# Kernel tuning notes

Measured on AMD Instinct MI355X. Metric: run time of the kernel, lower is better.

Reference implementation:

```python
import jax, jax.numpy as jnp
import numpy as np

N_NODES = 100000
N_EDGES = 3200000
F_IN = 128
NOUT = 32


def _lin(x, W, b):
    return x @ W + b


def _spect_conv(x, src, dst, W, b, n_nodes):
    # edge_attr is all-ones with a single frequency (K=1), so SpectConv reduces to
    # an unweighted scatter-add of linearly transformed source-node features.
    h = x @ W                                   # [N, nout]
    agg = jax.ops.segment_sum(h[src], dst, num_segments=n_nodes)  # [N, nout]
    return agg + b


def setup_inputs() -> dict:
    key = jax.random.key(0)
    ks = jax.random.split(key, 32)
    s = 0.05

    def w(k, shape):
        return jax.random.normal(k, shape, dtype=jnp.float32) * s

    inp = {
        "x": jax.random.normal(ks[0], (N_NODES, F_IN), dtype=jnp.float32),
        "edge_index": jax.random.randint(ks[1], (2, N_EDGES), 0, N_NODES, dtype=jnp.int32),
        # SpectConv weights (single frequency) + biases
        "Wc1": w(ks[2], (F_IN, NOUT)), "bc1": jnp.zeros((NOUT,), jnp.float32),
        "Wc2": w(ks[3], (NOUT, NOUT)), "bc2": jnp.zeros((NOUT,), jnp.float32),
        "Wc3": w(ks[4], (NOUT, NOUT)), "bc3": jnp.zeros((NOUT,), jnp.float32),
        # dense branch weights
        "W11": w(ks[5], (F_IN, NOUT)), "b11": w(ks[6], (NOUT,)),
        "W12": w(ks[7], (F_IN, NOUT)), "b12": w(ks[8], (NOUT,)),
        "W13": w(ks[9], (F_IN, NOUT)), "b13": w(ks[10], (NOUT,)),
        "W21": w(ks[11], (NOUT, NOUT)), "b21": w(ks[12], (NOUT,)),
        "W22": w(ks[13], (NOUT, NOUT)), "b22": w(ks[14], (NOUT,)),
        "W23": w(ks[15], (NOUT, NOUT)), "b23": w(ks[16], (NOUT,)),
        "W31": w(ks[17], (NOUT, NOUT)), "b31": w(ks[18], (NOUT,)),
        "W32": w(ks[19], (NOUT, NOUT)), "b32": w(ks[20], (NOUT,)),
        "W33": w(ks[21], (NOUT, NOUT)), "b33": w(ks[22], (NOUT,)),
        "W2": w(ks[23], (NOUT, 1)), "b2": w(ks[24], (1,)),
    }
    return inp


def reference(x, edge_index,
              Wc1, bc1, Wc2, bc2, Wc3, bc3,
              W11, b11, W12, b12, W13, b13,
              W21, b21, W22, b22, W23, b23,
              W31, b31, W32, b32, W33, b33,
              W2, b2):
    src, dst = edge_index[0], edge_index[1]
    n = x.shape[0]
    relu = jax.nn.relu

    def block(h, Wa, ba, Wc, bc, Wm1, bm1, Wm2, bm2):
        return (relu(_lin(h, Wa, ba))
                + relu(_spect_conv(h, src, dst, Wc, bc, n))
                + relu(_lin(h, Wm1, bm1) * _lin(h, Wm2, bm2)))

    h = block(x, W11, b11, Wc1, bc1, W12, b12, W13, b13)
    h = block(h, W21, b21, Wc2, bc2, W22, b22, W23, b23)
    h = block(h, W31, b31, Wc3, bc3, W32, b32, W33, b33)
    return _lin(h, W2, b2)
```

## Files before the change

kernel.cpp:

```cpp
#include <hip/hip_runtime.h>
#include <hip/hip_bf16.h>

#define N_FEAT 32
#define CBITS 7
#define CAP   6000
#define TILE  8192

typedef __attribute__((ext_vector_type(8))) short short8;
typedef __attribute__((ext_vector_type(4))) short short4e;
typedef __attribute__((ext_vector_type(4))) float floatx4;

static __device__ __forceinline__ unsigned short f2b(float f) {
    unsigned u = __float_as_uint(f);
    return (unsigned short)((u + 0x7FFFu + ((u >> 16) & 1u)) >> 16);
}
static __device__ __forceinline__ float b2f(unsigned short b) {
    return __uint_as_float(((unsigned)b) << 16);
}

template <int K, bool BF16_IN>
__global__ __launch_bounds__(256)
void transform_mfma_kernel(const void* __restrict__ hin,
                           const float* __restrict__ Wa, const float* __restrict__ ba,
                           const float* __restrict__ Wc,
                           const float* __restrict__ Wm1, const float* __restrict__ bm1,
                           const float* __restrict__ Wm2, const float* __restrict__ bm2,
                           unsigned short* __restrict__ t_pre, unsigned short* __restrict__ t_c,
                           int n_nodes)
{
    constexpr int WPITCH = (K == 32) ? 40 : 136;
    __shared__ unsigned short sW[128][WPITCH];

    const int t = threadIdx.x;
    const int node0 = blockIdx.x * 64;
    const int wave = t >> 6;
    const int lane = t & 63;
    const int m16 = lane & 15;
    const int quad = lane >> 4;

    for (int i = t; i < 128 * K; i += 256) {
        const int c = i & 127, kk = i >> 7;
        const int mat = c >> 5, cl = c & 31;
        const float* W = (mat == 0) ? Wa : (mat == 1) ? Wc : (mat == 2) ? Wm1 : Wm2;
        sW[c][kk] = f2b(W[(size_t)kk * 32 + cl]);
    }
    __syncthreads();

    const int n = node0 + wave * 16 + m16;
    const bool nok = (n < n_nodes);

    floatx4 acc[8];
#pragma unroll
    for (int i = 0; i < 8; ++i) acc[i] = (floatx4){0.f, 0.f, 0.f, 0.f};

#pragma unroll
    for (int k0 = 0; k0 < K; k0 += 32) {
        short8 a;
        if (BF16_IN) {
            const unsigned short* hb = (const unsigned short*)hin;
            a = nok ? *reinterpret_cast<const short8*>(hb + (size_t)n * K + k0 + quad * 8)
                    : (short8){0,0,0,0,0,0,0,0};
        } else {
            const float* hf = (const float*)hin;
            if (nok) {
                const float4 v0 = *reinterpret_cast<const float4*>(hf + (size_t)n * K + k0 + quad * 8);
                const float4 v1 = *reinterpret_cast<const float4*>(hf + (size_t)n * K + k0 + quad * 8 + 4);
                union { short8 v; unsigned short u[8]; } pk;
                pk.u[0] = f2b(v0.x); pk.u[1] = f2b(v0.y); pk.u[2] = f2b(v0.z); pk.u[3] = f2b(v0.w);
                pk.u[4] = f2b(v1.x); pk.u[5] = f2b(v1.y); pk.u[6] = f2b(v1.z); pk.u[7] = f2b(v1.w);
                a = pk.v;
            } else {
                a = (short8){0,0,0,0,0,0,0,0};
            }
        }
#pragma unroll
        for (int t8 = 0; t8 < 8; ++t8) {
            const short8 b = *reinterpret_cast<const short8*>(&sW[t8 * 16 + m16][k0 + quad * 8]);
            acc[t8] = __builtin_amdgcn_mfma_f32_16x16x32_bf16(a, b, acc[t8], 0, 0, 0);
        }
    }

#pragma unroll
    for (int r = 0; r < 4; ++r) {
        const int node = node0 + wave * 16 + quad * 4 + r;
        if (node < n_nodes) {
#pragma unroll
            for (int half = 0; half < 2; ++half) {
                const int c = m16 + half * 16;
                const float av  = acc[0 + half][r] + ba[c];
                const float wcv = acc[2 + half][r];
                const float m1  = acc[4 + half][r] + bm1[c];
                const float m2  = acc[6 + half][r] + bm2[c];
                t_pre[(size_t)node * N_FEAT + c] = f2b(fmaxf(av, 0.f) + fmaxf(m1 * m2, 0.f));
                t_c[(size_t)node * N_FEAT + c] = f2b(wcv);
            }
        }
    }
}

__global__ __launch_bounds__(1024)
void coarse_bin_kernel(const int* __restrict__ src, const int* __restrict__ dst,
                       unsigned* __restrict__ cnt_g, unsigned* __restrict__ binned,
                       int n_edges, int n_buckets)
{
    __shared__ unsigned sorted[TILE];
    __shared__ unsigned short buck[TILE];
    __shared__ unsigned hist[1024];
    __shared__ unsigned lbase[1024];
    __shared__ unsigned gofs[1024];
    __shared__ unsigned wsum[16], woff[16];

    const int t = threadIdx.x;
    const int wave = t >> 6, lane = t & 63;
    const int e0 = blockIdx.x * TILE;
    const int cnt = min(TILE, n_edges - e0);
    if (cnt <= 0) return;

    hist[t] = 0;
    __syncthreads();

    unsigned dv[TILE / 1024], sv[TILE / 1024];
    int nk = 0;
    for (int i = t; i < cnt; i += 1024, ++nk) {
        dv[nk] = (unsigned)dst[e0 + i];
        sv[nk] = (unsigned)src[e0 + i];
        atomicAdd(&hist[dv[nk] >> CBITS], 1u);
    }
    __syncthreads();

    const unsigned myh = hist[t];
    if (t < n_buckets)
        gofs[t] = myh ? atomicAdd(&cnt_g[t], myh) : 0u;

    unsigned v = myh;
#pragma unroll
    for (int off = 1; off < 64; off <<= 1) {
        const unsigned nv = __shfl_up(v, off);
        if (lane >= off) v += nv;
    }
    if (lane == 63) wsum[wave] = v;
    __syncthreads();
    if (t < 16) {
        unsigned s = wsum[t];
#pragma unroll
        for (int off = 1; off < 16; off <<= 1) {
            const unsigned nv = __shfl_up(s, off, 16);
            if (t >= off) s += nv;
        }
        woff[t] = s - wsum[t];
    }
    hist[t] = 0;
    __syncthreads();
    const unsigned lb_mine = v + woff[wave] - myh;
    lbase[t] = lb_mine;
    __syncthreads();

    for (int k = 0; k < nk; ++k) {
        const unsigned b = dv[k] >> CBITS;
        const unsigned pos = lbase[b] + atomicAdd(&hist[b], 1u);
        sorted[pos] = ((dv[k] & ((1u << CBITS) - 1)) << 17) | sv[k];
        buck[pos] = (unsigned short)b;
    }
    __syncthreads();

    for (int p = t; p < cnt; p += 1024) {
        const unsigned b = buck[p];
        const unsigned gp = gofs[b] + ((unsigned)p - lbase[b]);
        if (gp < CAP) binned[(size_t)b * CAP + gp] = sorted[p];
    }
}

__global__ __launch_bounds__(512)
void fine_sort_kernel(const unsigned* __restrict__ binned,
                      const unsigned* __restrict__ cnt_g,
                      unsigned* __restrict__ total_ctr,
                      int* __restrict__ srcs,
                      unsigned* __restrict__ rowstart, unsigned* __restrict__ rowend,
                      int n_nodes, int n_buckets)
{
    __shared__ int sorted_src[CAP];
    __shared__ unsigned hist[512];
    __shared__ unsigned incl[512];
    __shared__ unsigned ebase[512];
    __shared__ unsigned wsum[8], woff[8];
    __shared__ unsigned ob_s;

    const int t = threadIdx.x;
    const int wave = t >> 6, lane = t & 63;
    const int b = blockIdx.x;
    const unsigned cnt = min(cnt_g[b], (unsigned)CAP);
    const int node0 = b << CBITS;
    const int nodes_here = min(128, n_nodes - node0);
    const unsigned* tile = binned + (size_t)b * CAP;

    if (t == 0) ob_s = atomicAdd(total_ctr, cnt);
    hist[t] = 0;
    __syncthreads();
    const unsigned ob = ob_s;

    for (unsigned i = t; i < cnt; i += 512) {
        const unsigned e = tile[i];
        atomicAdd(&hist[((e >> 17) << 2) | ((e & 0x1FFFFu) >> 15)], 1u);
    }
    __syncthreads();

    const unsigned myh = hist[t];
    unsigned v = myh;
#pragma unroll
    for (int off = 1; off < 64; off <<= 1) {
        const unsigned nv = __shfl_up(v, off);
        if (lane >= off) v += nv;
    }
    if (lane == 63) wsum[wave] = v;
    __syncthreads();
    if (t < 8) {
        unsigned s = wsum[t];
#pragma unroll
        for (int off = 1; off < 8; off <<= 1) {
            const unsigned nv = __shfl_up(s, off, 8);
            if (t >= off) s += nv;
        }
        woff[t] = s - wsum[t];
    }
    hist[t] = 0;
    __syncthreads();
    const unsigned my_incl = v + woff[wave];
    incl[t] = my_incl;
    ebase[t] = my_incl - myh;
    __syncthreads();

    if (t < nodes_here) {
        rowstart[node0 + t] = ob + ebase[t << 2];
        rowend[node0 + t]   = ob + incl[(t << 2) + 3];
    }

    for (unsigned i = t; i < cnt; i += 512) {
        const unsigned e = tile[i];
        const unsigned key = ((e >> 17) << 2) | ((e & 0x1FFFFu) >> 15);
        const unsigned pos = ebase[key] + atomicAdd(&hist[key], 1u);
        sorted_src[pos] = (int)(e & 0x1FFFFu);
    }
    __syncthreads();
    for (unsigned i = t; i < cnt; i += 512)
        srcs[ob + i] = sorted_src[i];
}

static __device__ __forceinline__ void add4(float* a, short4e v) {
#pragma unroll
    for (int j = 0; j < 4; ++j) a[j] += b2f((unsigned short)v[j]);
}

__global__ __launch_bounds__(256)
void gather_combine_kernel(const unsigned short* __restrict__ t_c,
                           const unsigned short* __restrict__ t_pre,
                           const unsigned* __restrict__ rowstart,
                           const unsigned* __restrict__ rowend,
                           const int* __restrict__ srcs,
                           const float* __restrict__ bc, unsigned short* __restrict__ hout,
                           int n_nodes)
{
    const int node = blockIdx.x * 32 + (threadIdx.x >> 3);
    const int l8 = threadIdx.x & 7;
    const int f0 = l8 * 4;
    if (node >= n_nodes) return;
    const unsigned lo = rowstart[node], hi = rowend[node];
    float acc[4] = {0.f, 0.f, 0.f, 0.f};
    unsigned i = lo;

    if (i + 8 <= hi) {
        int sp[8];
#pragma unroll
        for (int j = 0; j < 8; ++j) sp[j] = srcs[i + j];
        for (;;) {
            short4e v[8];
#pragma unroll
            for (int j = 0; j < 8; ++j)
                v[j] = *reinterpret_cast<const short4e*>(t_c + (size_t)sp[j] * N_FEAT + f0);
            i += 8;
            const bool more = (i + 8 <= hi);
            int sn[8];
#pragma unroll
            for (int j = 0; j < 8; ++j) {
                const unsigned idx = more ? (i + j) : (hi - 1);
                sn[j] = srcs[idx];
            }
#pragma unroll
            for (int j = 0; j < 8; ++j) add4(acc, v[j]);
#pragma unroll
            for (int j = 0; j < 8; ++j) sp[j] = sn[j];
            if (!more) break;
        }
    }
    for (; i + 4 <= hi; i += 4) {
        short4e v[4];
#pragma unroll
        for (int j = 0; j < 4; ++j)
            v[j] = *reinterpret_cast<const short4e*>(t_c + (size_t)srcs[i + j] * N_FEAT + f0);
#pragma unroll
        for (int j = 0; j < 4; ++j) add4(acc, v[j]);
    }
    for (; i < hi; ++i)
        add4(acc, *reinterpret_cast<const short4e*>(t_c + (size_t)srcs[i] * N_FEAT + f0));

    const short4e p = *reinterpret_cast<const short4e*>(t_pre + (size_t)node * N_FEAT + f0);
    union { short4e v; unsigned short u[4]; } r;
#pragma unroll
    for (int j = 0; j < 4; ++j)
        r.u[j] = f2b(b2f((unsigned short)p[j]) + fmaxf(acc[j] + bc[f0 + j], 0.f));
    *reinterpret_cast<short4e*>(hout + (size_t)node * N_FEAT + f0) = r.v;
}

__global__ __launch_bounds__(256)
void gather_final_kernel(const unsigned short* __restrict__ t_c,
                         const unsigned short* __restrict__ t_pre,
                         const unsigned* __restrict__ rowstart,
                         const unsigned* __restrict__ rowend,
                         const int* __restrict__ srcs,
                         const float* __restrict__ bc, const float* __restrict__ W2,
                         const float* __restrict__ b2, float* __restrict__ out,
                         int n_nodes)
{
    const int node = blockIdx.x * 32 + (threadIdx.x >> 3);
    const int l8 = threadIdx.x & 7;
    const int f0 = l8 * 4;
    if (node >= n_nodes) return;
    const unsigned lo = rowstart[node], hi = rowend[node];
    float acc[4] = {0.f, 0.f, 0.f, 0.f};
    unsigned i = lo;

    if (i + 8 <= hi) {
        int sp[8];
#pragma unroll
        for (int j = 0; j < 8; ++j) sp[j] = srcs[i + j];
        for (;;) {
            short4e v[8];
#pragma unroll
            for (int j = 0; j < 8; ++j)
                v[j] = *reinterpret_cast<const short4e*>(t_c + (size_t)sp[j] * N_FEAT + f0);
            i += 8;
            const bool more = (i + 8 <= hi);
            int sn[8];
#pragma unroll
            for (int j = 0; j < 8; ++j) {
                const unsigned idx = more ? (i + j) : (hi - 1);
                sn[j] = srcs[idx];
            }
#pragma unroll
            for (int j = 0; j < 8; ++j) add4(acc, v[j]);
#pragma unroll
            for (int j = 0; j < 8; ++j) sp[j] = sn[j];
            if (!more) break;
        }
    }
    for (; i + 4 <= hi; i += 4) {
        short4e v[4];
#pragma unroll
        for (int j = 0; j < 4; ++j)
            v[j] = *reinterpret_cast<const short4e*>(t_c + (size_t)srcs[i + j] * N_FEAT + f0);
#pragma unroll
        for (int j = 0; j < 4; ++j) add4(acc, v[j]);
    }
    for (; i < hi; ++i)
        add4(acc, *reinterpret_cast<const short4e*>(t_c + (size_t)srcs[i] * N_FEAT + f0));

    const short4e p = *reinterpret_cast<const short4e*>(t_pre + (size_t)node * N_FEAT + f0);
    float r = 0.f;
#pragma unroll
    for (int j = 0; j < 4; ++j)
        r += (b2f((unsigned short)p[j]) + fmaxf(acc[j] + bc[f0 + j], 0.f)) * W2[f0 + j];
    r += __shfl_down(r, 4, 8);
    r += __shfl_down(r, 2, 8);
    r += __shfl_down(r, 1, 8);
    if (l8 == 0) out[node] = r + b2[0];
}

extern "C" void kernel_launch(void* const* d_in, const int* in_sizes, int n_in,
                              void* d_out, int out_size, void* d_ws, size_t ws_size,
                              hipStream_t stream)
{
    const float* x   = (const float*)d_in[0];
    const int*   ei  = (const int*)d_in[1];
    const float* Wc1 = (const float*)d_in[2];  const float* bc1 = (const float*)d_in[3];
    const float* Wc2 = (const float*)d_in[4];  const float* bc2 = (const float*)d_in[5];
    const float* Wc3 = (const float*)d_in[6];  const float* bc3 = (const float*)d_in[7];
    const float* W11 = (const float*)d_in[8];  const float* b11 = (const float*)d_in[9];
    const float* W12 = (const float*)d_in[10]; const float* b12 = (const float*)d_in[11];
    const float* W13 = (const float*)d_in[12]; const float* b13 = (const float*)d_in[13];
    const float* W21 = (const float*)d_in[14]; const float* b21 = (const float*)d_in[15];
    const float* W22 = (const float*)d_in[16]; const float* b22 = (const float*)d_in[17];
    const float* W23 = (const float*)d_in[18]; const float* b23 = (const float*)d_in[19];
    const float* W31 = (const float*)d_in[20]; const float* b31 = (const float*)d_in[21];
    const float* W32 = (const float*)d_in[22]; const float* b32 = (const float*)d_in[23];
    const float* W33 = (const float*)d_in[24]; const float* b33 = (const float*)d_in[25];
    const float* W2  = (const float*)d_in[26]; const float* b2  = (const float*)d_in[27];

    const int n_nodes = in_sizes[0] / 128;
    const int n_edges = in_sizes[1] / 2;
    const int* src = ei;
    const int* dst = ei + n_edges;
    const int n_buckets = (n_nodes + (1 << CBITS) - 1) >> CBITS;

    const size_t feat_elems = (size_t)n_nodes * N_FEAT;

    unsigned short* tpre     = (unsigned short*)d_ws;
    unsigned short* tc       = tpre + feat_elems;
    unsigned short* hbuf     = tc + feat_elems;
    int*            srcs     = (int*)(hbuf + feat_elems);
    unsigned*       rowstart = (unsigned*)(srcs + n_edges);
    unsigned*       rowend   = rowstart + n_nodes;
    unsigned*       cnt_g    = rowend + n_nodes;
    unsigned*       binned   = cnt_g + (n_buckets + 1);

    const int tf_grid = (n_nodes + 63) / 64;
    const int gc_grid = (n_nodes + 31) / 32;
    const int cb_grid = (n_edges + TILE - 1) / TILE;

    hipMemsetAsync(cnt_g, 0, ((size_t)n_buckets + 1) * sizeof(unsigned), stream);
    coarse_bin_kernel<<<cb_grid, 1024, 0, stream>>>(src, dst, cnt_g, binned, n_edges, n_buckets);
    fine_sort_kernel<<<n_buckets, 512, 0, stream>>>(
        binned, cnt_g, cnt_g + n_buckets, srcs, rowstart, rowend, n_nodes, n_buckets);

    transform_mfma_kernel<128, false><<<tf_grid, 256, 0, stream>>>(
        x, W11, b11, Wc1, W12, b12, W13, b13, tpre, tc, n_nodes);
    gather_combine_kernel<<<gc_grid, 256, 0, stream>>>(
        tc, tpre, rowstart, rowend, srcs, bc1, hbuf, n_nodes);

    transform_mfma_kernel<32, true><<<tf_grid, 256, 0, stream>>>(
        hbuf, W21, b21, Wc2, W22, b22, W23, b23, tpre, tc, n_nodes);
    gather_combine_kernel<<<gc_grid, 256, 0, stream>>>(
        tc, tpre, rowstart, rowend, srcs, bc2, hbuf, n_nodes);

    transform_mfma_kernel<32, true><<<tf_grid, 256, 0, stream>>>(
        hbuf, W31, b31, Wc3, W32, b32, W33, b33, tpre, tc, n_nodes);
    gather_final_kernel<<<gc_grid, 256, 0, stream>>>(
        tc, tpre, rowstart, rowend, srcs, bc3, W2, b2, (float*)d_out, n_nodes);
}
```

Before: 334.9 us.

## Fuse gather-combine with next layer's MFMA transform and ping-pong buffers

Merges the per-layer gather/combine kernel with the following layer's four-way linear transform into one kernel. Each 512-thread block gathers 64 nodes into shared memory, then four waves run bf16 MFMA on them. This removes the intermediate h write and read and two kernel launches per layer. Ping-pong tpre/tc buffers keep the next layer's inputs from being overwritten while other blocks still read them. In exchange, the weights are reloaded into shared memory per block and half the waves sit idle during the MFMA phase.

```diff
diff --git a/kernel.cpp b/kernel.cpp
--- a/kernel.cpp
+++ b/kernel.cpp
@@ -250,64 +250,125 @@
     for (int j = 0; j < 4; ++j) a[j] += b2f((unsigned short)v[j]);
 }
 
-__global__ __launch_bounds__(256)
-void gather_combine_kernel(const unsigned short* __restrict__ t_c,
-                           const unsigned short* __restrict__ t_pre,
-                           const unsigned* __restrict__ rowstart,
-                           const unsigned* __restrict__ rowend,
-                           const int* __restrict__ srcs,
-                           const float* __restrict__ bc, unsigned short* __restrict__ hout,
-                           int n_nodes)
-{
-    const int node = blockIdx.x * 32 + (threadIdx.x >> 3);
-    const int l8 = threadIdx.x & 7;
+__global__ __launch_bounds__(512)
+void gather_transform_kernel(const unsigned short* __restrict__ t_c_in,
+                             const unsigned short* __restrict__ t_pre_in,
+                             const unsigned* __restrict__ rowstart,
+                             const unsigned* __restrict__ rowend,
+                             const int* __restrict__ srcs,
+                             const float* __restrict__ bc,
+                             const float* __restrict__ Wa, const float* __restrict__ ba,
+                             const float* __restrict__ Wc,
+                             const float* __restrict__ Wm1, const float* __restrict__ bm1,
+                             const float* __restrict__ Wm2, const float* __restrict__ bm2,
+                             unsigned short* __restrict__ t_pre_out,
+                             unsigned short* __restrict__ t_c_out,
+                             int n_nodes)
+{
+    __shared__ unsigned short sW[128][40];
+    __shared__ unsigned short sH[64][40];
+
+    const int t = threadIdx.x;
+    const int node0 = blockIdx.x * 64;
+
+    for (int i = t; i < 128 * 32; i += 512) {
+        const int c = i & 127, kk = i >> 7;
+        const int mat = c >> 5, cl = c & 31;
+        const float* W = (mat == 0) ? Wa : (mat == 1) ? Wc : (mat == 2) ? Wm1 : Wm2;
+        sW[c][kk] = f2b(W[(size_t)kk * 32 + cl]);
+    }
+
+    const int nl = t >> 3;
+    const int node = node0 + nl;
+    const int l8 = t & 7;
     const int f0 = l8 * 4;
-    if (node >= n_nodes) return;
-    const unsigned lo = rowstart[node], hi = rowend[node];
-    float acc[4] = {0.f, 0.f, 0.f, 0.f};
-    unsigned i = lo;
-
-    if (i + 8 <= hi) {
-        int sp[8];
-#pragma unroll
-        for (int j = 0; j < 8; ++j) sp[j] = srcs[i + j];
-        for (;;) {
-            short4e v[8];
-#pragma unroll
-            for (int j = 0; j < 8; ++j)
-                v[j] = *reinterpret_cast<const short4e*>(t_c + (size_t)sp[j] * N_FEAT + f0);
-            i += 8;
-            const bool more = (i + 8 <= hi);
-            int sn[8];
-#pragma unroll
-            for (int j = 0; j < 8; ++j) {
-                const unsigned idx = more ? (i + j) : (hi - 1);
-                sn[j] = srcs[idx];
+    const bool nvalid = (node < n_nodes);
+
+    if (nvalid) {
+        const unsigned lo = rowstart[node], hi = rowend[node];
+        float acc[4] = {0.f, 0.f, 0.f, 0.f};
+        unsigned i = lo;
+
+        if (i + 8 <= hi) {
+            int sp[8];
+#pragma unroll
+            for (int j = 0; j < 8; ++j) sp[j] = srcs[i + j];
+            for (;;) {
+                short4e v[8];
+#pragma unroll
+                for (int j = 0; j < 8; ++j)
+                    v[j] = *reinterpret_cast<const short4e*>(t_c_in + (size_t)sp[j] * N_FEAT + f0);
+                i += 8;
+                const bool more = (i + 8 <= hi);
+                int sn[8];
+#pragma unroll
+                for (int j = 0; j < 8; ++j) {
+                    const unsigned idx = more ? (i + j) : (hi - 1);
+                    sn[j] = srcs[idx];
+                }
+#pragma unroll
+                for (int j = 0; j < 8; ++j) add4(acc, v[j]);
+#pragma unroll
+                for (int j = 0; j < 8; ++j) sp[j] = sn[j];
+                if (!more) break;
             }
-#pragma unroll
-            for (int j = 0; j < 8; ++j) add4(acc, v[j]);
-#pragma unroll
-            for (int j = 0; j < 8; ++j) sp[j] = sn[j];
-            if (!more) break;
-        }
-    }
-    for (; i + 4 <= hi; i += 4) {
-        short4e v[4];
+        }
+        for (; i + 4 <= hi; i += 4) {
+            short4e v[4];
+#pragma unroll
+            for (int j = 0; j < 4; ++j)
+                v[j] = *reinterpret_cast<const short4e*>(t_c_in + (size_t)srcs[i + j] * N_FEAT + f0);
+#pragma unroll
+            for (int j = 0; j < 4; ++j) add4(acc, v[j]);
+        }
+        for (; i < hi; ++i)
+            add4(acc, *reinterpret_cast<const short4e*>(t_c_in + (size_t)srcs[i] * N_FEAT + f0));
+
+        const short4e p = *reinterpret_cast<const short4e*>(t_pre_in + (size_t)node * N_FEAT + f0);
+        union { short4e v; unsigned short u[4]; } r;
 #pragma unroll
         for (int j = 0; j < 4; ++j)
-            v[j] = *reinterpret_cast<const short4e*>(t_c + (size_t)srcs[i + j] * N_FEAT + f0);
-#pragma unroll
-        for (int j = 0; j < 4; ++j) add4(acc, v[j]);
-    }
-    for (; i < hi; ++i)
-        add4(acc, *reinterpret_cast<const short4e*>(t_c + (size_t)srcs[i] * N_FEAT + f0));
-
-    const short4e p = *reinterpret_cast<const short4e*>(t_pre + (size_t)node * N_FEAT + f0);
-    union { short4e v; unsigned short u[4]; } r;
-#pragma unroll
-    for (int j = 0; j < 4; ++j)
-        r.u[j] = f2b(b2f((unsigned short)p[j]) + fmaxf(acc[j] + bc[f0 + j], 0.f));
-    *reinterpret_cast<short4e*>(hout + (size_t)node * N_FEAT + f0) = r.v;
+            r.u[j] = f2b(b2f((unsigned short)p[j]) + fmaxf(acc[j] + bc[f0 + j], 0.f));
+        *reinterpret_cast<short4e*>(&sH[nl][f0]) = r.v;
+    } else {
+        *reinterpret_cast<short4e*>(&sH[nl][f0]) = (short4e){0, 0, 0, 0};
+    }
+    __syncthreads();
+
+    const int wave = t >> 6;
+    if (wave < 4) {
+        const int lane = t & 63;
+        const int m16 = lane & 15;
+        const int quad = lane >> 4;
+
+        floatx4 acc2[8];
+#pragma unroll
+        for (int i = 0; i < 8; ++i) acc2[i] = (floatx4){0.f, 0.f, 0.f, 0.f};
+
+        const short8 a = *reinterpret_cast<const short8*>(&sH[wave * 16 + m16][quad * 8]);
+#pragma unroll
+        for (int t8 = 0; t8 < 8; ++t8) {
+            const short8 b = *reinterpret_cast<const short8*>(&sW[t8 * 16 + m16][quad * 8]);
+            acc2[t8] = __builtin_amdgcn_mfma_f32_16x16x32_bf16(a, b, acc2[t8], 0, 0, 0);
+        }
+
+#pragma unroll
+        for (int r = 0; r < 4; ++r) {
+            const int onode = node0 + wave * 16 + quad * 4 + r;
+            if (onode < n_nodes) {
+#pragma unroll
+                for (int half = 0; half < 2; ++half) {
+                    const int c = m16 + half * 16;
+                    const float av  = acc2[0 + half][r] + ba[c];
+                    const float wcv = acc2[2 + half][r];
+                    const float m1  = acc2[4 + half][r] + bm1[c];
+                    const float m2  = acc2[6 + half][r] + bm2[c];
+                    t_pre_out[(size_t)onode * N_FEAT + c] = f2b(fmaxf(av, 0.f) + fmaxf(m1 * m2, 0.f));
+                    t_c_out[(size_t)onode * N_FEAT + c] = f2b(wcv);
+                }
+            }
+        }
+    }
 }
 
 __global__ __launch_bounds__(256)
@@ -402,17 +463,19 @@
 
     const size_t feat_elems = (size_t)n_nodes * N_FEAT;
 
-    unsigned short* tpre     = (unsigned short*)d_ws;
-    unsigned short* tc       = tpre + feat_elems;
-    unsigned short* hbuf     = tc + feat_elems;
-    int*            srcs     = (int*)(hbuf + feat_elems);
+    unsigned short* tpreA    = (unsigned short*)d_ws;
+    unsigned short* tcA      = tpreA + feat_elems;
+    unsigned short* tpreB    = tcA + feat_elems;
+    unsigned short* tcB      = tpreB + feat_elems;
+    int*            srcs     = (int*)(tcB + feat_elems);
     unsigned*       rowstart = (unsigned*)(srcs + n_edges);
     unsigned*       rowend   = rowstart + n_nodes;
     unsigned*       cnt_g    = rowend + n_nodes;
     unsigned*       binned   = cnt_g + (n_buckets + 1);
 
     const int tf_grid = (n_nodes + 63) / 64;
-    const int gc_grid = (n_nodes + 31) / 32;
+    const int gt_grid = (n_nodes + 63) / 64;
+    const int gf_grid = (n_nodes + 31) / 32;
     const int cb_grid = (n_edges + TILE - 1) / TILE;
 
     hipMemsetAsync(cnt_g, 0, ((size_t)n_buckets + 1) * sizeof(unsigned), stream);
@@ -421,17 +484,16 @@
         binned, cnt_g, cnt_g + n_buckets, srcs, rowstart, rowend, n_nodes, n_buckets);
 
     transform_mfma_kernel<128, false><<<tf_grid, 256, 0, stream>>>(
-        x, W11, b11, Wc1, W12, b12, W13, b13, tpre, tc, n_nodes);
-    gather_combine_kernel<<<gc_grid, 256, 0, stream>>>(
-        tc, tpre, rowstart, rowend, srcs, bc1, hbuf, n_nodes);
-
-    transform_mfma_kernel<32, true><<<tf_grid, 256, 0, stream>>>(
-        hbuf, W21, b21, Wc2, W22, b22, W23, b23, tpre, tc, n_nodes);
-    gather_combine_kernel<<<gc_grid, 256, 0, stream>>>(
-        tc, tpre, rowstart, rowend, srcs, bc2, hbuf, n_nodes);
-
-    transform_mfma_kernel<32, true><<<tf_grid, 256, 0, stream>>>(
-        hbuf, W31, b31, Wc3, W32, b32, W33, b33, tpre, tc, n_nodes);
-    gather_final_kernel<<<gc_grid, 256, 0, stream>>>(
-        tc, tpre, rowstart, rowend, srcs, bc3, W2, b2, (float*)d_out, n_nodes);
-}
+        x, W11, b11, Wc1, W12, b12, W13, b13, tpreA, tcA, n_nodes);
+
+    gather_transform_kernel<<<gt_grid, 512, 0, stream>>>(
+        tcA, tpreA, rowstart, rowend, srcs, bc1,
+        W21, b21, Wc2, W22, b22, W23, b23, tpreB, tcB, n_nodes);
+
+    gather_transform_kernel<<<gt_grid, 512, 0, stream>>>(
+        tcB, tpreB, rowstart, rowend, srcs, bc2,
+        W31, b31, Wc3, W32, b32, W33, b33, tpreA, tcA, n_nodes);
+
+    gather_final_kernel<<<gf_grid, 256, 0, stream>>>(
+        tcA, tpreA, rowstart, rowend, srcs, bc3, W2, b2, (float*)d_out, n_nodes);
+}
```

Result: faster. 321.8 us (-3.9%).
